# Performance work log

Measured on AMD Instinct MI355X. Metric: run time of the kernel, lower is better.

The kernel has to match this reference:

```python
import jax, jax.numpy as jnp
import numpy as np
from jax import lax

B, H, W, C = 8, 128, 128, 256
HEADS, DHEAD = 8, 32
INNER = HEADS * DHEAD  # == C, required by pos_emb reshape


def setup_inputs() -> dict:
    key = jax.random.key(0)
    ks = jax.random.split(key, 12)
    s = 0.02
    return {
        "x_in": jax.random.normal(ks[0], (B, H, W, C), jnp.float32),
        "Wq": jax.random.normal(ks[1], (INNER, C), jnp.float32) * s,
        "Wk": jax.random.normal(ks[2], (INNER, C), jnp.float32) * s,
        "Wv": jax.random.normal(ks[3], (INNER, C), jnp.float32) * s,
        "rescale": jnp.ones((HEADS, 1, 1), jnp.float32),
        "Wp": jax.random.normal(ks[4], (C, INNER), jnp.float32) * s,
        "bp": jnp.zeros((C,), jnp.float32),
        "Wc1": jax.random.normal(ks[5], (INNER, INNER, 3, 3), jnp.float32) * s,
        "bc1": jnp.zeros((INNER,), jnp.float32),
        "Wc2": jax.random.normal(ks[6], (INNER, INNER, 3, 3), jnp.float32) * s,
        "bc2": jnp.zeros((INNER,), jnp.float32),
    }


def _l2norm(x, axis=-1, eps=1e-12):
    n = jnp.sqrt(jnp.sum(x * x, axis=axis, keepdims=True))
    return x / jnp.maximum(n, eps)


def _conv(x, w, b):
    y = lax.conv_general_dilated(x, w, (1, 1), 'SAME',
                                 dimension_numbers=('NCHW', 'OIHW', 'NCHW'))
    return y + b[None, :, None, None]


def reference(x_in, Wq, Wk, Wv, rescale, Wp, bp, Wc1, bc1, Wc2, bc2):
    b, h, w, c = x_in.shape
    n = h * w
    x = x_in.reshape(b, n, c)
    q_inp = x @ Wq.T  # [b, n, inner]
    k_inp = x @ Wk.T
    v_inp = x @ Wv.T

    def heads(t):  # b n (h d) -> b h d n  (already transposed)
        return t.reshape(b, n, HEADS, DHEAD).transpose(0, 2, 3, 1)

    q = _l2norm(heads(q_inp))  # [b, heads, d, n], normalized over n
    k = _l2norm(heads(k_inp))
    v = heads(v_inp)  # [b, heads, d, n]

    attn = jnp.einsum('bhdn,bhen->bhde', k, q) * rescale  # [b, heads, d, d]
    attn = jax.nn.softmax(attn, axis=-1)
    xo = jnp.einsum('bhde,bhen->bhdn', attn, v)  # [b, heads, d, n]
    xo = xo.transpose(0, 3, 1, 2).reshape(b, n, INNER)  # b n (heads d)
    out_c = (xo @ Wp.T + bp).reshape(b, h, w, c)

    vp = v_inp.reshape(b, h, w, INNER).transpose(0, 3, 1, 2)  # NCHW
    p = _conv(vp, Wc1, bc1)
    p = jax.nn.gelu(p, approximate=False)
    p = _conv(p, Wc2, bc2)
    out_p = p.transpose(0, 2, 3, 1)  # b h w c
    return out_c, out_p
```

## Files before the change

### kernel.cpp

```cpp
#include <hip/hip_runtime.h>
#include <cstdint>

#define DEV __device__ __forceinline__

typedef __bf16 bf16x8 __attribute__((ext_vector_type(8)));
typedef float f32x4 __attribute__((ext_vector_type(4)));
typedef unsigned int u32;
typedef unsigned short u16;

DEV u16 f2bf(float f) {
  u32 u = __builtin_bit_cast(u32, f);
  u += 0x7fffu + ((u >> 16) & 1u);
  return (u16)(u >> 16);
}
DEV float bf2f(u16 b) { return __builtin_bit_cast(float, (u32)b << 16); }

DEV void gload16(const u16* g, u16* l) {
  __builtin_amdgcn_global_load_lds(
      (const __attribute__((address_space(1))) u32*)g,
      (__attribute__((address_space(3))) u32*)(uintptr_t)l, 16, 0, 0);
}

DEV void border_body(u16* __restrict__ p, int idx) {
  int pix = idx >> 5, c8 = (idx & 31) << 3;
  int b = pix / 516, r = pix % 516;
  int x, y;
  if (r < 130)      { y = 0;   x = r; }
  else if (r < 260) { y = 129; x = r - 130; }
  else if (r < 388) { x = 0;   y = r - 259; }
  else              { x = 129; y = r - 387; }
  u16* dst = p + (((long)b * 130 + y) * 130 + x) * 256 + c8;
  *reinterpret_cast<uint4*>(dst) = uint4{0, 0, 0, 0};
}

__global__ void cvt_f32_bf16(const float* __restrict__ in, u16* __restrict__ out, int n4) {
  int i = blockIdx.x * blockDim.x + threadIdx.x;
  if (i >= n4) return;
  float4 v = reinterpret_cast<const float4*>(in)[i];
  ushort4 o;
  o.x = f2bf(v.x); o.y = f2bf(v.y); o.z = f2bf(v.z); o.w = f2bf(v.w);
  reinterpret_cast<ushort4*>(out)[i] = o;
}

__global__ void prep(const float* __restrict__ Wq, const float* __restrict__ Wk,
                     const float* __restrict__ Wv, const float* __restrict__ Wc1,
                     const float* __restrict__ Wc2, u16* __restrict__ wqkv,
                     u16* __restrict__ wc1r, u16* __restrict__ wc2r, u16* __restrict__ vpad) {
  const int blk = blockIdx.x, t = threadIdx.x;
  if (blk < 192) {
    const float* src = blk < 64 ? Wq : (blk < 128 ? Wk : Wv);
    u16* dst = wqkv + (blk < 64 ? 0 : (blk < 128 ? 65536 : 131072));
    const int i = (blk & 63) * 256 + t;
    float4 v = reinterpret_cast<const float4*>(src)[i];
    ushort4 o;
    o.x = f2bf(v.x); o.y = f2bf(v.y); o.z = f2bf(v.z); o.w = f2bf(v.w);
    reinterpret_cast<ushort4*>(dst)[i] = o;
  } else if (blk < 4800) {
    const int q = blk - 192;
    const float* w = q < 2304 ? Wc1 : Wc2;
    u16* dst = q < 2304 ? wc1r : wc2r;
    const int j = (q % 2304) * 256 + t;
    const int oc = j / 2304, r = j - oc * 2304;
    const int kt = r >> 6, c_lo = r & 63;
    const int cg = kt / 9, slab = kt - cg * 9;
    const int ic = cg * 64 + c_lo;
    dst[j] = f2bf(w[(oc * 256 + ic) * 9 + slab]);
  } else {
    const int idx = (blk - 4800) * 256 + t;
    if (idx < 8 * 516 * 32) border_body(vpad, idx);
  }
}

template <int CONV, int KTOT, int EPI, int PERB, int SWZ>
__global__ __launch_bounds__(512, 1) void mm8(
    const u16* __restrict__ A, const u16* __restrict__ Bt,
    const float* __restrict__ bias, void* __restrict__ out,
    u16* __restrict__ vp) {
  extern __shared__ u16 lds[];
  constexpr int NKT = KTOT / 64;
  constexpr int NITER = NKT / 2;
  const int tid = threadIdx.x;
  const int wave = tid >> 6, lane = tid & 63;
  const int wr = wave >> 2, wcid = wave & 3;
  const int lrow = lane & 15, lk = lane >> 4;
  int bid = (int)blockIdx.x;
  int tile, colbase;
  if (SWZ == 1) {
    const int xcd = bid & 7, k = bid >> 3;
    tile = (xcd + ((k >> 5) << 3)) * 32 + (k & 31);
    colbase = 0;
  } else if (SWZ == 2) {
    const int xcd = bid & 7, s = bid >> 3;
    const int r = s / 3;
    tile = xcd * 64 + r;
    colbase = (s - r * 3) * 256;
  } else {
    tile = (bid & 7) * 64 + (bid >> 3);
    colbase = 0;
  }
  const long rowbase = (long)tile * 256;
  const int bimg = tile >> 6;
  const int y0 = (tile & 63) * 2;
  const u16* BT = PERB ? Bt + (long)bimg * 65536 : Bt;

  auto STAGE = [&](int kt, int isB, int half, int bufq) {
#pragma unroll
    for (int j = 0; j < 2; ++j) {
      const int idx = j * 512 + tid;
      const int rh = idx >> 3;
      const int sg = (idx & 7) ^ (rh & 7);
      const u16* g;
      if (isB) {
        g = BT + (long)(colbase + half * 128 + rh) * KTOT + kt * 64 + sg * 8;
      } else if (CONV == 1) {
        const int cg = kt / 9;
        const int slab = kt - cg * 9;
        const int ky = slab / 3 - 1, kx = slab - (slab / 3) * 3 - 1;
        const int c0 = cg * 64;
        g = A + (((long)bimg * 130 + (y0 + half) + 1 + ky) * 130 + (rh + 1 + kx)) * 256 + c0 + sg * 8;
      } else if (CONV == 2) {
        g = A + (((long)bimg * 130 + (y0 + half) + 1) * 130 + (rh + 1)) * 256 + kt * 64 + sg * 8;
      } else {
        g = A + (rowbase + half * 128 + rh) * (long)256 + kt * 64 + sg * 8;
      }
      u16* l = lds + (isB ? 32768 : 0) + bufq * 16384 + half * 8192 + (j * 512 + wave * 64) * 8;
      gload16(g, l);
    }
  };

  f32x4 acc[8][4] = {};
  bf16x8 bq[4][2];

  STAGE(0, 1, 0, 0); STAGE(0, 1, 1, 0);
  STAGE(0, 0, 0, 0); STAGE(0, 0, 1, 0);
  STAGE(1, 1, 0, 1); STAGE(1, 1, 1, 1);
  asm volatile("s_waitcnt vmcnt(4)" ::: "memory");
  __builtin_amdgcn_s_barrier();
  __builtin_amdgcn_sched_barrier(0);

  for (int it = 0; it < NITER; ++it) {
    const int u0 = 2 * it;
#pragma unroll
    for (int ph = 0; ph < 8; ++ph) {
      constexpr int S_ISB[8]  = {0, 0, 1, 1, 0, 0, 1, 1};
      constexpr int S_HALF[8] = {0, 1, 0, 1, 0, 1, 0, 1};
      constexpr int S_BUF[8]  = {1, 1, 0, 0, 0, 0, 1, 1};
      constexpr int S_DT[8]   = {1, 1, 2, 2, 2, 2, 3, 3};
      const int cbuf = ph >> 2, quad = ph & 3;
      if (quad == 0) {
#pragma unroll
        for (int nf = 0; nf < 4; ++nf)
#pragma unroll
          for (int ks = 0; ks < 2; ++ks) {
            const int n = wcid * 64 + nf * 16 + lrow;
            const int slot = (ks * 4 + lk) ^ (n & 7);
            bq[nf][ks] = *reinterpret_cast<const bf16x8*>(&lds[32768 + cbuf * 16384 + n * 64 + slot * 8]);
          }
      }
      bf16x8 aq[2][2];
#pragma unroll
      for (int mf = 0; mf < 2; ++mf)
#pragma unroll
        for (int ks = 0; ks < 2; ++ks) {
          const int r = wr * 128 + quad * 32 + mf * 16 + lrow;
          const int slot = (ks * 4 + lk) ^ (r & 7);
          aq[mf][ks] = *reinterpret_cast<const bf16x8*>(&lds[cbuf * 16384 + r * 64 + slot * 8]);
        }
      int st = u0 + S_DT[ph];
      if (st > NKT - 1) st = NKT - 1;
      STAGE(st, S_ISB[ph], S_HALF[ph], S_BUF[ph]);
      if (quad == 0)
        asm volatile("s_waitcnt lgkmcnt(8)" ::: "memory");
      __builtin_amdgcn_s_barrier();
      asm volatile("s_waitcnt lgkmcnt(0)" ::: "memory");
      __builtin_amdgcn_sched_barrier(0);
      __builtin_amdgcn_s_setprio(1);
#pragma unroll
      for (int mf = 0; mf < 2; ++mf)
#pragma unroll
        for (int nf = 0; nf < 4; ++nf)
#pragma unroll
          for (int ks = 0; ks < 2; ++ks)
            acc[quad * 2 + mf][nf] = __builtin_amdgcn_mfma_f32_16x16x32_bf16(
                aq[mf][ks], bq[nf][ks], acc[quad * 2 + mf][nf], 0, 0, 0);
      __builtin_amdgcn_s_setprio(0);
      __builtin_amdgcn_sched_barrier(0);
      if (quad == 3)
        asm volatile("s_waitcnt vmcnt(4)" ::: "memory");
      __builtin_amdgcn_s_barrier();
      __builtin_amdgcn_sched_barrier(0);
    }
  }

  const int r0 = (lane >> 4) * 4;
  const int occ = lane & 15;
#pragma unroll
  for (int M = 0; M < 8; ++M) {
#pragma unroll
    for (int nf = 0; nf < 4; ++nf) {
      const int col = wcid * 64 + nf * 16 + occ;
#pragma unroll
      for (int i = 0; i < 4; ++i) {
        const int p = wr * 128 + M * 16 + r0 + i;
        float v = acc[M][nf][i];
        if (EPI == 0) {
          const long rowpix = rowbase + p;
          const int gcol = colbase + col;
          if (gcol < 512) {
            reinterpret_cast<u16*>(out)[rowpix * 512 + gcol] = f2bf(v);
          } else {
            const int b = (int)(rowpix >> 14), rem = (int)(rowpix & 16383);
            vp[(((long)b * 130 + (rem >> 7) + 1) * 130 + (rem & 127) + 1) * 256 + (gcol - 512)] = f2bf(v);
          }
        } else if (EPI == 1) {
          reinterpret_cast<float*>(out)[(rowbase + p) * 256 + col] = v + bias[col];
        } else {
          v += bias[col];
          v = 0.5f * v * (1.0f + erff(v * 0.70710678118654752f));
          const int y = y0 + (p >> 7), x = p & 127;
          reinterpret_cast<u16*>(out)[(((long)bimg * 130 + y + 1) * 130 + x + 1) * 256 + col] = f2bf(v);
        }
      }
    }
  }
}

__global__ __launch_bounds__(256) void gram_kernel(const u16* __restrict__ qkv,
                                                   float* __restrict__ G,
                                                   float* __restrict__ norm2) {
  const int chunk = blockIdx.x;
  const int bh = blockIdx.y;
  const int b = bh >> 3, h = bh & 7;
  __shared__ float kk[32][33];
  __shared__ float qq[32][33];
  const int tid = threadIdx.x;
  const int rr = tid >> 3;
  const int c4 = (tid & 7) * 4;
  const long rowstart = (long)b * 16384 + (long)chunk * 2048;
  const u16* qp = qkv + rowstart * 512 + h * 32;
  const u16* kp = qp + 256;
  float acc0 = 0, acc1 = 0, acc2 = 0, acc3 = 0;
  float skk[4] = {0, 0, 0, 0}, sqq[4] = {0, 0, 0, 0};
  for (int t0 = 0; t0 < 2048; t0 += 32) {
    __syncthreads();
    ushort4 kv = *reinterpret_cast<const ushort4*>(kp + (long)(t0 + rr) * 512 + c4);
    ushort4 qv = *reinterpret_cast<const ushort4*>(qp + (long)(t0 + rr) * 512 + c4);
    float f;
    f = bf2f(kv.x); kk[rr][c4 + 0] = f; skk[0] += f * f;
    f = bf2f(kv.y); kk[rr][c4 + 1] = f; skk[1] += f * f;
    f = bf2f(kv.z); kk[rr][c4 + 2] = f; skk[2] += f * f;
    f = bf2f(kv.w); kk[rr][c4 + 3] = f; skk[3] += f * f;
    f = bf2f(qv.x); qq[rr][c4 + 0] = f; sqq[0] += f * f;
    f = bf2f(qv.y); qq[rr][c4 + 1] = f; sqq[1] += f * f;
    f = bf2f(qv.z); qq[rr][c4 + 2] = f; sqq[2] += f * f;
    f = bf2f(qv.w); qq[rr][c4 + 3] = f; sqq[3] += f * f;
    __syncthreads();
#pragma unroll
    for (int r = 0; r < 32; ++r) {
      const float kval = kk[r][rr];
      acc0 += kval * qq[r][c4 + 0];
      acc1 += kval * qq[r][c4 + 1];
      acc2 += kval * qq[r][c4 + 2];
      acc3 += kval * qq[r][c4 + 3];
    }
  }
  float* gp = G + ((long)bh * 32 + rr) * 32 + c4;
  atomicAdd(gp + 0, acc0); atomicAdd(gp + 1, acc1);
  atomicAdd(gp + 2, acc2); atomicAdd(gp + 3, acc3);
  __syncthreads();
  kk[rr][c4 + 0] = skk[0]; kk[rr][c4 + 1] = skk[1];
  kk[rr][c4 + 2] = skk[2]; kk[rr][c4 + 3] = skk[3];
  qq[rr][c4 + 0] = sqq[0]; qq[rr][c4 + 1] = sqq[1];
  qq[rr][c4 + 2] = sqq[2]; qq[rr][c4 + 3] = sqq[3];
  __syncthreads();
  if (tid < 64) {
    const int col = tid & 31;
    float s = 0.f;
    if (tid < 32) {
#pragma unroll
      for (int r2 = 0; r2 < 32; ++r2) s += kk[r2][col];
      atomicAdd(&norm2[b * 512 + 256 + h * 32 + col], s);
    } else {
#pragma unroll
      for (int r2 = 0; r2 < 32; ++r2) s += qq[r2][col];
      atomicAdd(&norm2[b * 512 + h * 32 + col], s);
    }
  }
}

__global__ void attn_softmax(const float* __restrict__ G, const float* __restrict__ norm2,
                             const float* __restrict__ rescale, float* __restrict__ attn) {
  const int bh = blockIdx.x;
  const int b = bh >> 3, h = bh & 7;
  const int t = threadIdx.x;
  __shared__ float iqs[32], iks[32];
  if (t < 32) {
    iqs[t] = 1.0f / fmaxf(sqrtf(norm2[b * 512 + h * 32 + t]), 1e-12f);
    iks[t] = 1.0f / fmaxf(sqrtf(norm2[b * 512 + 256 + h * 32 + t]), 1e-12f);
  }
  __syncthreads();
  if (t < 32) {
    const float rs = rescale[h];
    const float ikd = iks[t] * rs;
    const float* gp = G + ((long)bh * 32 + t) * 32;
    float l[32];
    float mx = -1e30f;
#pragma unroll
    for (int e = 0; e < 32; ++e) {
      l[e] = gp[e] * ikd * iqs[e];
      mx = fmaxf(mx, l[e]);
    }
    float s = 0.f;
#pragma unroll
    for (int e = 0; e < 32; ++e) {
      l[e] = expf(l[e] - mx);
      s += l[e];
    }
    const float inv = 1.0f / s;
    float* op = attn + ((long)bh * 32 + t) * 32;
#pragma unroll
    for (int e = 0; e < 32; ++e) op[e] = l[e] * inv;
  }
}

__global__ __launch_bounds__(256) void weff_border(const float* __restrict__ Wp,
                                                   const float* __restrict__ attn,
                                                   u16* __restrict__ weff,
                                                   u16* __restrict__ p1pad) {
  const int blk = blockIdx.x;
  const int t = threadIdx.x;
  if (blk < 64) {
    __shared__ float A[32][33];
    const int b = blk >> 3, h = blk & 7;
    const float* ap = attn + (long)blk * 1024;
    for (int j = t; j < 1024; j += 256) A[j >> 5][j & 31] = ap[j];
    __syncthreads();
    const float* wrow = Wp + (long)t * 256 + h * 32;
    float w[32];
#pragma unroll
    for (int d = 0; d < 32; ++d) w[d] = wrow[d];
    u16* orow = weff + ((long)b * 256 + t) * 256 + h * 32;
#pragma unroll
    for (int e = 0; e < 32; ++e) {
      float s = 0.f;
#pragma unroll
      for (int d = 0; d < 32; ++d) s += w[d] * A[d][e];
      orow[e] = f2bf(s);
    }
  } else {
    const int idx = (blk - 64) * 256 + t;
    if (idx < 8 * 516 * 32) border_body(p1pad, idx);
  }
}

extern "C" void kernel_launch(void* const* d_in, const int* in_sizes, int n_in,
                              void* d_out, int out_size, void* d_ws, size_t ws_size,
                              hipStream_t stream) {
  const float* x = (const float*)d_in[0];
  const float* Wq = (const float*)d_in[1];
  const float* Wk = (const float*)d_in[2];
  const float* Wv = (const float*)d_in[3];
  const float* resc = (const float*)d_in[4];
  const float* Wp = (const float*)d_in[5];
  const float* bp = (const float*)d_in[6];
  const float* Wc1 = (const float*)d_in[7];
  const float* bc1 = (const float*)d_in[8];
  const float* Wc2 = (const float*)d_in[9];
  const float* bc2 = (const float*)d_in[10];

  char* ws = (char*)d_ws;
  u16* qkv   = (u16*)(ws + 0L);
  u16* p1pad = (u16*)(ws + 0L);
  u16* vpad  = (u16*)(ws + 134217728L);
  u16* xb    = (u16*)(ws + 203440128L);
  u16* wqkv  = (u16*)(ws + 270548992L);
  u16* wc1r  = (u16*)(ws + 270942208L);
  u16* wc2r  = (u16*)(ws + 272121856L);
  u16* weff  = (u16*)(ws + 273301504L);
  float* norm2 = (float*)(ws + 274350080L);
  float* G     = (float*)(ws + 274366464L);
  float* attn  = (float*)(ws + 274628608L);

  float* out_c = (float*)d_out;
  float* out_p = out_c + 33554432L;

  hipMemsetAsync(norm2, 0, 16384 + 262144, stream);

  cvt_f32_bf16<<<32768, 256, 0, stream>>>(x, xb, 8388608);
  prep<<<5316, 256, 0, stream>>>(Wq, Wk, Wv, Wc1, Wc2, wqkv, wc1r, wc2r, vpad);

  mm8<0, 256, 0, 0, 2><<<1536, 512, 131072, stream>>>(xb, wqkv, nullptr, qkv, vpad);

  gram_kernel<<<dim3(8, 64), 256, 0, stream>>>(qkv, G, norm2);
  attn_softmax<<<64, 64, 0, stream>>>(G, norm2, resc, attn);
  weff_border<<<580, 256, 0, stream>>>(Wp, attn, weff, p1pad);

  mm8<2, 256, 1, 1, 0><<<512, 512, 131072, stream>>>(vpad, weff, bp, out_c, nullptr);

  mm8<1, 2304, 2, 0, 1><<<512, 512, 131072, stream>>>(vpad, wc1r, bc1, p1pad, nullptr);
  mm8<1, 2304, 1, 0, 1><<<512, 512, 131072, stream>>>(p1pad, wc2r, bc2, out_p, nullptr);
}
```

Baseline: 625.1 us.

## Use MFMA for the Gram reduction and vectorize GEMM epilogue stores

Replaces the scalar fp32 Gram kernel with an MFMA-based version. It transposes q/k tiles into double-buffered LDS and register-prefetches the next chunks, with half as many blocks, each covering a longer sequence range. The GEMM epilogues now use lane shuffles to pack four adjacent columns, so one lane per group issues a 16-byte or 8-byte store instead of four scalar stores. This trades extra shuffles and idle lanes during stores for fewer, wider memory transactions. In the new Gram kernel each 32-row step does only one small MFMA per wave, behind a barrier.

```diff
diff --git a/kernel.cpp b/kernel.cpp
--- a/kernel.cpp
+++ b/kernel.cpp
@@ -199,92 +199,125 @@
 #pragma unroll
     for (int nf = 0; nf < 4; ++nf) {
       const int col = wcid * 64 + nf * 16 + occ;
+      const int col4 = col & ~3;
 #pragma unroll
       for (int i = 0; i < 4; ++i) {
         const int p = wr * 128 + M * 16 + r0 + i;
         float v = acc[M][nf][i];
-        if (EPI == 0) {
-          const long rowpix = rowbase + p;
-          const int gcol = colbase + col;
-          if (gcol < 512) {
-            reinterpret_cast<u16*>(out)[rowpix * 512 + gcol] = f2bf(v);
-          } else {
-            const int b = (int)(rowpix >> 14), rem = (int)(rowpix & 16383);
-            vp[(((long)b * 130 + (rem >> 7) + 1) * 130 + (rem & 127) + 1) * 256 + (gcol - 512)] = f2bf(v);
+        if (EPI == 1) {
+          v += bias[col];
+          float s1 = __shfl_xor(v, 1);
+          float s2 = __shfl_xor(v, 2);
+          float s3 = __shfl_xor(s1, 2);
+          if ((lane & 3) == 0)
+            *reinterpret_cast<float4*>(reinterpret_cast<float*>(out) + (rowbase + p) * 256 + col4) =
+                float4{v, s1, s2, s3};
+        } else {
+          if (EPI == 2) {
+            v += bias[col];
+            v = 0.5f * v * (1.0f + erff(v * 0.70710678118654752f));
           }
-        } else if (EPI == 1) {
-          reinterpret_cast<float*>(out)[(rowbase + p) * 256 + col] = v + bias[col];
-        } else {
-          v += bias[col];
-          v = 0.5f * v * (1.0f + erff(v * 0.70710678118654752f));
-          const int y = y0 + (p >> 7), x = p & 127;
-          reinterpret_cast<u16*>(out)[(((long)bimg * 130 + y + 1) * 130 + x + 1) * 256 + col] = f2bf(v);
+          u32 me = f2bf(v);
+          u32 n1 = (u32)__shfl_xor((int)me, 1);
+          u32 pair = (lane & 1) ? ((me << 16) | n1) : (me | (n1 << 16));
+          u32 p2 = (u32)__shfl_xor((int)pair, 2);
+          if ((lane & 3) == 0) {
+            if (EPI == 2) {
+              const int y = y0 + (p >> 7), x = p & 127;
+              *reinterpret_cast<uint2*>(reinterpret_cast<u16*>(out) +
+                  (((long)bimg * 130 + y + 1) * 130 + x + 1) * 256 + col4) = uint2{pair, p2};
+            } else {
+              const int gcol4 = colbase + col4;
+              const long rowpix = rowbase + p;
+              if (gcol4 < 512) {
+                *reinterpret_cast<uint2*>(reinterpret_cast<u16*>(out) + rowpix * 512 + gcol4) =
+                    uint2{pair, p2};
+              } else {
+                const int b_ = (int)(rowpix >> 14), rem = (int)(rowpix & 16383);
+                *reinterpret_cast<uint2*>(vp + (((long)b_ * 130 + (rem >> 7) + 1) * 130 +
+                    (rem & 127) + 1) * 256 + (gcol4 - 512)) = uint2{pair, p2};
+              }
+            }
+          }
         }
       }
     }
   }
 }
 
-__global__ __launch_bounds__(256) void gram_kernel(const u16* __restrict__ qkv,
-                                                   float* __restrict__ G,
-                                                   float* __restrict__ norm2) {
-  const int chunk = blockIdx.x;
+__global__ __launch_bounds__(256) void gram_mfma(const u16* __restrict__ qkv,
+                                                 float* __restrict__ G,
+                                                 float* __restrict__ norm2) {
+  __shared__ __align__(16) u16 kT[2][32][40];
+  __shared__ __align__(16) u16 qT[2][32][40];
+  __shared__ float redq[256][4];
+  __shared__ float redk[256][4];
+  const int nc = blockIdx.x;
   const int bh = blockIdx.y;
   const int b = bh >> 3, h = bh & 7;
-  __shared__ float kk[32][33];
-  __shared__ float qq[32][33];
-  const int tid = threadIdx.x;
-  const int rr = tid >> 3;
-  const int c4 = (tid & 7) * 4;
-  const long rowstart = (long)b * 16384 + (long)chunk * 2048;
-  const u16* qp = qkv + rowstart * 512 + h * 32;
+  const int t = threadIdx.x;
+  const int wave = t >> 6, lane = t & 63;
+  const int mh = wave >> 1, nh = wave & 1;
+  const int r = t >> 3, cg = (t & 7) * 4;
+  const long n0 = (long)b * 16384 + (long)nc * 4096;
+  const u16* qp = qkv + n0 * 512 + h * 32;
   const u16* kp = qp + 256;
-  float acc0 = 0, acc1 = 0, acc2 = 0, acc3 = 0;
-  float skk[4] = {0, 0, 0, 0}, sqq[4] = {0, 0, 0, 0};
-  for (int t0 = 0; t0 < 2048; t0 += 32) {
-    __syncthreads();
-    ushort4 kv = *reinterpret_cast<const ushort4*>(kp + (long)(t0 + rr) * 512 + c4);
-    ushort4 qv = *reinterpret_cast<const ushort4*>(qp + (long)(t0 + rr) * 512 + c4);
-    float f;
-    f = bf2f(kv.x); kk[rr][c4 + 0] = f; skk[0] += f * f;
-    f = bf2f(kv.y); kk[rr][c4 + 1] = f; skk[1] += f * f;
-    f = bf2f(kv.z); kk[rr][c4 + 2] = f; skk[2] += f * f;
-    f = bf2f(kv.w); kk[rr][c4 + 3] = f; skk[3] += f * f;
-    f = bf2f(qv.x); qq[rr][c4 + 0] = f; sqq[0] += f * f;
-    f = bf2f(qv.y); qq[rr][c4 + 1] = f; sqq[1] += f * f;
-    f = bf2f(qv.z); qq[rr][c4 + 2] = f; sqq[2] += f * f;
-    f = bf2f(qv.w); qq[rr][c4 + 3] = f; sqq[3] += f * f;
-    __syncthreads();
-#pragma unroll
-    for (int r = 0; r < 32; ++r) {
-      const float kval = kk[r][rr];
-      acc0 += kval * qq[r][c4 + 0];
-      acc1 += kval * qq[r][c4 + 1];
-      acc2 += kval * qq[r][c4 + 2];
-      acc3 += kval * qq[r][c4 + 3];
-    }
-  }
-  float* gp = G + ((long)bh * 32 + rr) * 32 + c4;
-  atomicAdd(gp + 0, acc0); atomicAdd(gp + 1, acc1);
-  atomicAdd(gp + 2, acc2); atomicAdd(gp + 3, acc3);
+  f32x4 acc = {0.f, 0.f, 0.f, 0.f};
+  float sq[4] = {0, 0, 0, 0}, sk[4] = {0, 0, 0, 0};
+
+  ushort4 pq[4], pk[4];
+#pragma unroll
+  for (int j = 0; j < 4; ++j) {
+    pq[j] = *reinterpret_cast<const ushort4*>(qp + (long)(j * 32 + r) * 512 + cg);
+    pk[j] = *reinterpret_cast<const ushort4*>(kp + (long)(j * 32 + r) * 512 + cg);
+  }
+
+  for (int s4 = 0; s4 < 32; ++s4) {
+#pragma unroll
+    for (int c = 0; c < 4; ++c) {
+      const int s = s4 * 4 + c;
+      const int buf = s & 1;
+      kT[buf][cg + 0][r] = pk[c].x; kT[buf][cg + 1][r] = pk[c].y;
+      kT[buf][cg + 2][r] = pk[c].z; kT[buf][cg + 3][r] = pk[c].w;
+      qT[buf][cg + 0][r] = pq[c].x; qT[buf][cg + 1][r] = pq[c].y;
+      qT[buf][cg + 2][r] = pq[c].z; qT[buf][cg + 3][r] = pq[c].w;
+      float f;
+      f = bf2f(pq[c].x); sq[0] += f * f;
+      f = bf2f(pq[c].y); sq[1] += f * f;
+      f = bf2f(pq[c].z); sq[2] += f * f;
+      f = bf2f(pq[c].w); sq[3] += f * f;
+      f = bf2f(pk[c].x); sk[0] += f * f;
+      f = bf2f(pk[c].y); sk[1] += f * f;
+      f = bf2f(pk[c].z); sk[2] += f * f;
+      f = bf2f(pk[c].w); sk[3] += f * f;
+      if (s + 4 < 128) {
+        pq[c] = *reinterpret_cast<const ushort4*>(qp + (long)((s + 4) * 32 + r) * 512 + cg);
+        pk[c] = *reinterpret_cast<const ushort4*>(kp + (long)((s + 4) * 32 + r) * 512 + cg);
+      }
+      __syncthreads();
+      bf16x8 af = *reinterpret_cast<const bf16x8*>(&kT[buf][mh * 16 + (lane & 15)][(lane >> 4) * 8]);
+      bf16x8 bf = *reinterpret_cast<const bf16x8*>(&qT[buf][nh * 16 + (lane & 15)][(lane >> 4) * 8]);
+      acc = __builtin_amdgcn_mfma_f32_16x16x32_bf16(af, bf, acc, 0, 0, 0);
+    }
+  }
+
+  float* gp = G + (long)bh * 1024 + (mh * 16 + (lane >> 4) * 4) * 32 + nh * 16 + (lane & 15);
+#pragma unroll
+  for (int i = 0; i < 4; ++i) atomicAdd(gp + i * 32, acc[i]);
+
   __syncthreads();
-  kk[rr][c4 + 0] = skk[0]; kk[rr][c4 + 1] = skk[1];
-  kk[rr][c4 + 2] = skk[2]; kk[rr][c4 + 3] = skk[3];
-  qq[rr][c4 + 0] = sqq[0]; qq[rr][c4 + 1] = sqq[1];
-  qq[rr][c4 + 2] = sqq[2]; qq[rr][c4 + 3] = sqq[3];
+#pragma unroll
+  for (int j = 0; j < 4; ++j) { redq[t][j] = sq[j]; redk[t][j] = sk[j]; }
   __syncthreads();
-  if (tid < 64) {
-    const int col = tid & 31;
+  if (t < 64) {
+    const int qk = t >> 5;
+    const int colid = t & 31;
+    const int cgi = colid >> 2, j = colid & 3;
     float s = 0.f;
-    if (tid < 32) {
-#pragma unroll
-      for (int r2 = 0; r2 < 32; ++r2) s += kk[r2][col];
-      atomicAdd(&norm2[b * 512 + 256 + h * 32 + col], s);
-    } else {
-#pragma unroll
-      for (int r2 = 0; r2 < 32; ++r2) s += qq[r2][col];
-      atomicAdd(&norm2[b * 512 + h * 32 + col], s);
-    }
+#pragma unroll
+    for (int r2 = 0; r2 < 32; ++r2)
+      s += qk ? redk[r2 * 8 + cgi][j] : redq[r2 * 8 + cgi][j];
+    atomicAdd(&norm2[b * 512 + qk * 256 + h * 32 + colid], s);
   }
 }
 
@@ -391,7 +424,7 @@
 
   mm8<0, 256, 0, 0, 2><<<1536, 512, 131072, stream>>>(xb, wqkv, nullptr, qkv, vpad);
 
-  gram_kernel<<<dim3(8, 64), 256, 0, stream>>>(qkv, G, norm2);
+  gram_mfma<<<dim3(4, 64), 256, 0, stream>>>(qkv, G, norm2);
   attn_softmax<<<64, 64, 0, stream>>>(G, norm2, resc, attn);
   weff_border<<<580, 256, 0, stream>>>(Wp, attn, weff, p1pad);
 
```

New measurement: 629.2 us. Within noise of the previous version (+0.6%).
